# Optimization experiments

Hardware: AMD Instinct MI355X
Metric: run time of the kernel (lower is better)

Reference implementation:

```python
import jax, jax.numpy as jnp
import numpy as np

N_QUBITS = 8
REPS = 2
DIM = 2 ** N_QUBITS  # 256
C64 = jnp.complex64


def _apply_1q(state, gate, wire):
    """Apply a single-qubit gate. state: [B]+[2]*n, gate: [2,2] or [B,2,2]."""
    s = jnp.moveaxis(state, wire + 1, -1)
    if gate.ndim == 2:
        s = jnp.einsum('ij,b...j->b...i', gate, s)
    else:
        s = jnp.einsum('bij,b...j->b...i', gate, s)
    return jnp.moveaxis(s, -1, wire + 1)


def _cnot(state, ctrl, tgt):
    """CNOT: flip target axis where control bit == 1. state: [B]+[2]*n."""
    s0 = jax.lax.index_in_dim(state, 0, ctrl + 1, keepdims=True)
    s1 = jax.lax.index_in_dim(state, 1, ctrl + 1, keepdims=True)
    s1 = jnp.flip(s1, axis=tgt + 1)
    return jnp.concatenate([s0, s1], axis=ctrl + 1)


def _rx(a):
    """Batched RX gate. a: [B] -> [B,2,2] complex64."""
    c = jnp.cos(0.5 * a).astype(C64)
    s = jnp.sin(0.5 * a).astype(C64)
    mis = (-1j) * s
    return jnp.stack([jnp.stack([c, mis], -1), jnp.stack([mis, c], -1)], -2)


def _rot(phi, theta, omega):
    """PennyLane Rot = RZ(omega) RY(theta) RZ(phi). Scalars -> [2,2] complex64."""
    c = jnp.cos(0.5 * theta).astype(C64)
    s = jnp.sin(0.5 * theta).astype(C64)
    ep = jnp.exp(-0.5j * (phi + omega).astype(C64))   # e^{-i(phi+omega)/2}
    em = jnp.exp(-0.5j * (phi - omega).astype(C64))   # e^{-i(phi-omega)/2}
    epc = jnp.exp(0.5j * (phi + omega).astype(C64))
    emc = jnp.exp(0.5j * (phi - omega).astype(C64))
    return jnp.stack([
        jnp.stack([ep * c, -emc * s], -1),
        jnp.stack([em * s, epc * c], -1),
    ], -2)


def _circuit(x, theta):
    B = x.shape[0]
    state = jnp.zeros((B, DIM), C64).at[:, 0].set(1.0)
    state = state.reshape((B,) + (2,) * N_QUBITS)
    # AngleEmbedding (default rotation='X'): RX(x[:, w]) on wire w
    for w in range(N_QUBITS):
        state = _apply_1q(state, _rx(x[:, w]), w)
    # StronglyEntanglingLayers: per layer, Rot on every wire then ring of CNOTs
    for l in range(REPS):
        for w in range(N_QUBITS):
            g = _rot(theta[l, w, 0], theta[l, w, 1], theta[l, w, 2])
            state = _apply_1q(state, g, w)
        r = (l % (N_QUBITS - 1)) + 1  # PennyLane default ranges
        for w in range(N_QUBITS):
            state = _cnot(state, w, (w + r) % N_QUBITS)
    # expval(PauliZ(0)): wire 0 is the most significant axis
    probs = (state.real ** 2 + state.imag ** 2).reshape(B, 2, DIM // 2)
    ev = probs[:, 0].sum(-1) - probs[:, 1].sum(-1)
    return ((ev + 1.0) * 0.5)[:, None]  # [B, 1]


def setup_inputs() -> dict:
    key = jax.random.key(0)
    kx, kt = jax.random.split(key)
    x = jax.random.normal(kx, (131072, N_QUBITS), dtype=jnp.float32)
    theta = 0.1 * jax.random.normal(kt, (REPS, N_QUBITS, 3), dtype=jnp.float32)
    return {"x": x, "theta": theta}


def reference(x, theta):
    return _circuit(x, theta)
```

## Files before the change

### kernel.cpp

```cpp
#include <hip/hip_runtime.h>


typedef _Float16 v8hf __attribute__((ext_vector_type(8)));
typedef float v4f __attribute__((ext_vector_type(4)));

struct cpx { float re, im; };
__device__ __forceinline__ cpx cmul(cpx a, cpx b) {
    return {a.re * b.re - a.im * b.im, a.re * b.im + a.im * b.re};
}

__device__ __forceinline__ cpx pget(int a, int i, int j) {
    static const float RE[4][4] = {{1, 0, 0, 1}, {0, 1, 1, 0},
                                   {0, 0, 0, 0}, {1, 0, 0, -1}};
    static const float IM[4][4] = {{0, 0, 0, 0}, {0, 0, 0, 0},
                                   {0, -1, 1, 0}, {0, 0, 0, 0}};
    cpx r; r.re = RE[a][i * 2 + j]; r.im = IM[a][i * 2 + j];
    return r;
}

__device__ float ptm_entry(const float* __restrict__ theta, int g, int a, int b) {
    const int l = g >> 3, w = g & 7;
    const float phi = theta[(l * 8 + w) * 3 + 0];
    const float th  = theta[(l * 8 + w) * 3 + 1];
    const float om  = theta[(l * 8 + w) * 3 + 2];
    const float c = cosf(0.5f * th), s = sinf(0.5f * th);
    const float ps = 0.5f * (phi + om), ms = 0.5f * (phi - om);
    cpx G[2][2];
    G[0][0] = {c * cosf(ps), -c * sinf(ps)};
    G[0][1] = {-s * cosf(ms), -s * sinf(ms)};
    G[1][0] = {s * cosf(ms), -s * sinf(ms)};
    G[1][1] = {c * cosf(ps), c * sinf(ps)};
    cpx M1[2][2], H[2][2];
#pragma unroll
    for (int i = 0; i < 2; ++i)
#pragma unroll
        for (int j = 0; j < 2; ++j) {
            cpx acc{0.f, 0.f};
#pragma unroll
            for (int k = 0; k < 2; ++k) {
                cpx t = cmul(pget(a, i, k), G[k][j]);
                acc.re += t.re; acc.im += t.im;
            }
            M1[i][j] = acc;
        }
#pragma unroll
    for (int i = 0; i < 2; ++i)
#pragma unroll
        for (int j = 0; j < 2; ++j) {
            cpx acc{0.f, 0.f};
#pragma unroll
            for (int k = 0; k < 2; ++k) {
                cpx gc{G[k][i].re, -G[k][i].im};
                cpx t = cmul(gc, M1[k][j]);
                acc.re += t.re; acc.im += t.im;
            }
            H[i][j] = acc;
        }
    float tr = 0.f;
#pragma unroll
    for (int i = 0; i < 2; ++i)
#pragma unroll
        for (int j = 0; j < 2; ++j) {
            cpx pb = pget(b, i, j);
            tr += pb.re * H[j][i].re - pb.im * H[j][i].im;
        }
    return 0.5f * tr;
}

__device__ void cnot_entry(int pr, int cand, int* CIDX, float* CSGN) {
    const int pc = pr >> 2, pt = pr & 3;
    const int a = cand >> 2, b2 = cand & 3;
    const int perm[4] = {0, 1, 3, 2};
    float ov = 0.f;
#pragma unroll
    for (int r = 0; r < 4; ++r)
#pragma unroll
        for (int c2 = 0; c2 < 4; ++c2) {
            const int rp = perm[r], cp = perm[c2];
            cpx Rv = cmul(pget(pc, rp >> 1, cp >> 1), pget(pt, rp & 1, cp & 1));
            cpx Kv = cmul(pget(a, r >> 1, c2 >> 1), pget(b2, r & 1, c2 & 1));
            ov += Kv.re * Rv.re + Kv.im * Rv.im;
        }
    ov *= 0.25f;
    if (ov > 0.5f) { CIDX[pr] = cand; CSGN[pr] = 1.f; }
    else if (ov < -0.5f) { CIDX[pr] = cand; CSGN[pr] = -1.f; }
}

__device__ __forceinline__ int ring_conj_reg(int cur, int r,
                                             unsigned long long ci,
                                             unsigned cs, int& par) {
    for (int w = 7; w >= 0; --w) {
        const int tw = (w + r) & 7;
        const int pc = (cur >> (2 * w)) & 3;
        const int pt = (cur >> (2 * tw)) & 3;
        const int q = pc * 4 + pt;
        const int nq = (int)((ci >> (4 * q)) & 15ULL);
        par ^= (int)((cs >> q) & 1u);
        cur = (cur & ~((3 << (2 * w)) | (3 << (2 * tw))))
            | ((nq >> 2) << (2 * w)) | ((nq & 3) << (2 * tw));
    }
    return cur;
}

#define WS_FLOATS_NEEDED 6912

__global__ __launch_bounds__(1024) void k_prep4(const float* __restrict__ theta,
                                                float* __restrict__ ws) {
    _Float16* AF16 = (_Float16*)ws;
    const int tid = threadIdx.x;
    const int blk = blockIdx.x;

    if (blk == 9) {
        for (int h = tid; h < 27 * 64 * 8; h += 1024) {
            const int L = (h >> 3) & 63;
            const int jj = h & 7;
            const int m = L & 15;
            const int j = (L >> 4) * 8 + jj;
            const bool valid = (m < 12) && ((m & 3) < 3) && (j < 27);
            if (!valid) AF16[h] = (_Float16)0.f;
        }
        return;
    }

    __shared__ float Wa[4096];
    __shared__ float Wb[3072];
    __shared__ float TR[256];
    __shared__ float CSGN[16];
    __shared__ int   CIDX[16];
    __shared__ int   S1k, S1n;
    __shared__ float S1sgn;
    __shared__ int   S1w[8], S1l[8];

    const int P0 = blk / 3, P1 = blk % 3;
    const int let0 = (P0 == 0) ? 0 : ((P0 == 1) ? 3 : 2);
    const int let1 = (P1 == 0) ? 0 : ((P1 == 1) ? 3 : 2);

    if (tid < 256) TR[tid] = ptm_entry(theta, tid >> 4, (tid >> 2) & 3, tid & 3);
    else if (tid < 512) {
        const int r = tid - 256;
        cnot_entry(r >> 4, r & 15, CIDX, CSGN);
    }
    for (int i = tid; i < 4096; i += 1024) Wa[i] = 0.f;
    __syncthreads();

    unsigned long long cidx_pk = 0ULL;
    unsigned csgn_pk = 0u;
#pragma unroll
    for (int i2 = 0; i2 < 16; ++i2) {
        cidx_pk |= (unsigned long long)(CIDX[i2] & 15) << (4 * i2);
        csgn_pk |= (CSGN[i2] < 0.f ? 1u : 0u) << i2;
    }

    if (tid == 0) {
        int par = 0;
        int cur = ring_conj_reg(3 , 2, cidx_pk, csgn_pk, par);
        int k = 0;
        for (int w = 0; w < 8; ++w) {
            const int ltr = (cur >> (2 * w)) & 3;
            if (ltr != 0) { S1w[k] = w; S1l[k] = ltr; ++k; }
        }
        int n = 1;
        for (int i = 0; i < k; ++i) n *= 3;
        S1sgn = par ? -1.f : 1.f; S1k = k; S1n = n;
    }
    __syncthreads();
    const int k1 = S1k, n1 = S1n;

    for (int t = tid; t < n1; t += 1024) {
        float c = S1sgn;
        int s = 0;
        int tt = t;
        for (int i = 0; i < k1; ++i) {
            const int bl = tt % 3 + 1;
            tt /= 3;
            c *= TR[(8 + S1w[i]) * 16 + S1l[i] * 4 + bl];
            s |= bl << (2 * S1w[i]);
        }
        int par = 0;
        s = ring_conj_reg(s, 1, cidx_pk, csgn_pk, par);
        c = par ? -c : c;
        const int a0 = s & 3, a1 = (s >> 2) & 3;
        int d4 = 0;
#pragma unroll
        for (int w = 2; w < 8; ++w)
            d4 |= ((s >> (2 * w)) & 3) << (2 * (7 - w));
        const float v = c * TR[a0 * 4 + let0] * TR[16 + a1 * 4 + let1];
        atomicAdd(&Wa[d4], v);
    }
    __syncthreads();

    const int P3c[6] = {1, 3, 9, 27, 81, 243};
    const int N4c[6] = {1024, 256, 64, 16, 4, 1};
#pragma unroll
    for (int tl = 0; tl < 6; ++tl) {
        const int w = 7 - tl;
        const float* src = (tl & 1) ? Wb : Wa;
        float* dst = (tl & 1) ? Wa : Wb;
        const int p3 = P3c[tl];
        const int Nout = p3 * 3 * N4c[tl];
        for (int idx = tid; idx < Nout; idx += 1024) {
            const int q3 = idx % p3;
            const int rest = idx / p3;
            const int P = rest % 3;
            const int r = rest / 3;
            const int let = (P == 0) ? 0 : ((P == 1) ? 3 : 2);
            const float* ib = src + q3 + p3 * 4 * r;
            dst[idx] = ib[0] * TR[w * 16 + 0 + let]
                     + ib[p3] * TR[w * 16 + 4 + let]
                     + ib[2 * p3] * TR[w * 16 + 8 + let]
                     + ib[3 * p3] * TR[w * 16 + 12 + let];
        }
        __syncthreads();
    }

    const int m = 4 * P0 + P1;
    for (int idx = tid; idx < 729; idx += 1024) {
        const int T = idx / 27, j = idx % 27;
        const int h = (T * 64 + (j >> 3) * 16 + m) * 8 + (j & 7);
        AF16[h] = (_Float16)Wa[idx];
    }
}

__global__ __launch_bounds__(256) void k_main8(const float* __restrict__ x,
                                               const int* __restrict__ wsAF,
                                               float* __restrict__ out,
                                               int ngroups) {
    __shared__ int AFl[6912];
    const int tid = threadIdx.x;
    for (int u = tid; u < 6912; u += 256) AFl[u] = wsAF[u];
    __syncthreads();

    const int lane = tid & 63;
    const int q = lane >> 4, e = lane & 15;
    const bool q0b = (q == 0), q1b = (q == 1), q2b = (q == 2);
    const v8hf* AFp = (const v8hf*)AFl;
    const int wave = blockIdx.x * 4 + (tid >> 6);

#pragma unroll 1
    for (int gi = 0; gi < 2; ++gi) {
        const int g = wave * 2 + gi;
        if (g >= ngroups) break;
        const int b = g * 16 + e;
        const float4* xp = (const float4*)(x + (size_t)b * 8);
        const float4 xa = xp[0], xb = xp[1];

        float cw[8], msw[8];
        {
            const float xv[8] = {xa.x, xa.y, xa.z, xa.w, xb.x, xb.y, xb.z, xb.w};
#pragma unroll
            for (int w = 0; w < 8; ++w) {
                float sv, cv;
                __sincosf(xv[w], &sv, &cv);
                cw[w] = cv;
                msw[w] = -sv;
            }
        }

        float F2[27];
        {
            const float m5v[3] = {1.f, cw[5], msw[5]};
            const float m6v[3] = {1.f, cw[6], msw[6]};
            const float m7v[3] = {1.f, cw[7], msw[7]};
#pragma unroll
            for (int a = 0; a < 3; ++a)
#pragma unroll
                for (int b2 = 0; b2 < 3; ++b2) {
                    const float pp = m5v[a] * m6v[b2];
#pragma unroll
                    for (int c2 = 0; c2 < 3; ++c2)
                        F2[(a * 3 + b2) * 3 + c2] = pp * m7v[c2];
                }
        }
        v8hf bf;
#pragma unroll
        for (int jj = 0; jj < 8; ++jj) {
            const float c0 = F2[jj];
            const float c1 = F2[jj + 8];
            const float c2 = F2[jj + 16];
            const float c3 = (jj < 3) ? F2[jj + 24] : 0.f;
            const float v = q0b ? c0 : (q1b ? c1 : (q2b ? c2 : c3));
            bf[jj] = (_Float16)v;
        }

        const v4f zero = {0.f, 0.f, 0.f, 0.f};
        float h[9];
#pragma unroll
        for (int t = 0; t < 27; ++t) {
            const int a = t / 9, b2 = (t / 3) % 3, c2 = t % 3;
            v4f acc = __builtin_amdgcn_mfma_f32_16x16x32_f16(
                AFp[t * 64 + lane], bf, zero, 0, 0, 0);
            float f = fmaf(cw[1], acc[1], acc[0]);
            f = fmaf(msw[1], acc[2], f);
            if (c2 == 0)      h[a * 3 + b2] = f;
            else if (c2 == 1) h[a * 3 + b2] = fmaf(cw[4], f, h[a * 3 + b2]);
            else              h[a * 3 + b2] = fmaf(msw[4], f, h[a * 3 + b2]);
        }
        float e0 = fmaf(cw[3], h[1], h[0]); e0 = fmaf(msw[3], h[2], e0);
        float e1 = fmaf(cw[3], h[4], h[3]); e1 = fmaf(msw[3], h[5], e1);
        float e2 = fmaf(cw[3], h[7], h[6]); e2 = fmaf(msw[3], h[8], e2);
        float ev = fmaf(cw[2], e1, e0);
        ev = fmaf(msw[2], e2, ev);
        const float g0 = q0b ? 1.f : (q1b ? cw[0] : (q2b ? msw[0] : 0.f));
        ev *= g0;

        ev += __shfl_xor(ev, 16, 64);
        ev += __shfl_xor(ev, 32, 64);
        if (lane < 16) out[b] = (ev + 1.f) * 0.5f;
    }
}

struct c32 { float x, y; };

__device__ __forceinline__ c32 shfl_xor_c(c32 v, int mask) {
    c32 r;
    r.x = __shfl_xor(v.x, mask, 64);
    r.y = __shfl_xor(v.y, mask, 64);
    return r;
}
__device__ __forceinline__ c32 cmadd2(c32 ga, c32 a, c32 gp, c32 p) {
    c32 n;
    n.x = ga.x * a.x - ga.y * a.y + gp.x * p.x - gp.y * p.y;
    n.y = ga.x * a.y + ga.y * a.x + gp.x * p.y + gp.y * p.x;
    return n;
}
__device__ __forceinline__ c32 rx_mix(float c, float s, c32 a, c32 p) {
    c32 n;
    n.x = c * a.x + s * p.y;
    n.y = c * a.y - s * p.x;
    return n;
}
__device__ __forceinline__ void apply_rx(c32 st[4], int lane, int bb, float c, float s) {
    if (bb < 6) {
#pragma unroll
        for (int r = 0; r < 4; ++r) {
            c32 p = shfl_xor_c(st[r], 1 << bb);
            st[r] = rx_mix(c, s, st[r], p);
        }
    } else if (bb == 6) {
        c32 n0 = rx_mix(c, s, st[0], st[1]);
        c32 n1 = rx_mix(c, s, st[1], st[0]);
        c32 n2 = rx_mix(c, s, st[2], st[3]);
        c32 n3 = rx_mix(c, s, st[3], st[2]);
        st[0] = n0; st[1] = n1; st[2] = n2; st[3] = n3;
    } else {
        c32 n0 = rx_mix(c, s, st[0], st[2]);
        c32 n2 = rx_mix(c, s, st[2], st[0]);
        c32 n1 = rx_mix(c, s, st[1], st[3]);
        c32 n3 = rx_mix(c, s, st[3], st[1]);
        st[0] = n0; st[1] = n1; st[2] = n2; st[3] = n3;
    }
}
__device__ __forceinline__ void apply_rot(c32 st[4], int lane, int bb,
                                          c32 g00, c32 g01, c32 g10, c32 g11) {
    if (bb < 6) {
#pragma unroll
        for (int r = 0; r < 4; ++r) {
            c32 p = shfl_xor_c(st[r], 1 << bb);
            bool hi = (lane >> bb) & 1;
            c32 ga, gp;
            ga.x = hi ? g11.x : g00.x;
            ga.y = hi ? g11.y : g00.y;
            gp.x = hi ? g10.x : g01.x;
            gp.y = hi ? g10.y : g01.y;
            st[r] = cmadd2(ga, st[r], gp, p);
        }
    } else if (bb == 6) {
        c32 n0 = cmadd2(g00, st[0], g01, st[1]);
        c32 n1 = cmadd2(g10, st[0], g11, st[1]);
        c32 n2 = cmadd2(g00, st[2], g01, st[3]);
        c32 n3 = cmadd2(g10, st[2], g11, st[3]);
        st[0] = n0; st[1] = n1; st[2] = n2; st[3] = n3;
    } else {
        c32 n0 = cmadd2(g00, st[0], g01, st[2]);
        c32 n2 = cmadd2(g10, st[0], g11, st[2]);
        c32 n1 = cmadd2(g00, st[1], g01, st[3]);
        c32 n3 = cmadd2(g10, st[1], g11, st[3]);
        st[0] = n0; st[1] = n1; st[2] = n2; st[3] = n3;
    }
}
__device__ __forceinline__ void cswap(bool c, c32& a, c32& b) {
    c32 t = a;
    a.x = c ? b.x : a.x; a.y = c ? b.y : a.y;
    b.x = c ? t.x : b.x; b.y = c ? t.y : b.y;
}
__device__ __forceinline__ void apply_cnot(c32 st[4], int lane, int bc, int bt) {
    if (bt < 6) {
        if (bc < 6) {
            bool ctrl = (lane >> bc) & 1;
#pragma unroll
            for (int r = 0; r < 4; ++r) {
                c32 p = shfl_xor_c(st[r], 1 << bt);
                st[r].x = ctrl ? p.x : st[r].x;
                st[r].y = ctrl ? p.y : st[r].y;
            }
        } else {
#pragma unroll
            for (int r = 0; r < 4; ++r) {
                if ((r >> (bc - 6)) & 1) st[r] = shfl_xor_c(st[r], 1 << bt);
            }
        }
    } else {
        if (bc < 6) {
            bool ctrl = (lane >> bc) & 1;
            if (bt == 6) { cswap(ctrl, st[0], st[1]); cswap(ctrl, st[2], st[3]); }
            else         { cswap(ctrl, st[0], st[2]); cswap(ctrl, st[1], st[3]); }
        } else {
            if (bc == 7 && bt == 6) { c32 t = st[2]; st[2] = st[3]; st[3] = t; }
            else if (bc == 6 && bt == 7) { c32 t = st[1]; st[1] = st[3]; st[3] = t; }
        }
    }
}
__global__ __launch_bounds__(256) void qsim_kernel(const float* __restrict__ x,
                                                   const float* __restrict__ theta,
                                                   float* __restrict__ out,
                                                   int batch) {
    __shared__ float rot[2 * 8 * 8];
    const int t = threadIdx.x;
    if (t < 16) {
        const int l = t >> 3, w = t & 7;
        const float phi = theta[(l * 8 + w) * 3 + 0];
        const float th  = theta[(l * 8 + w) * 3 + 1];
        const float om  = theta[(l * 8 + w) * 3 + 2];
        const float c = cosf(0.5f * th), s = sinf(0.5f * th);
        const float p = 0.5f * (phi + om), m = 0.5f * (phi - om);
        float* g = &rot[t * 8];
        g[0] = c * cosf(p);  g[1] = -c * sinf(p);
        g[2] = -s * cosf(m); g[3] = -s * sinf(m);
        g[4] = s * cosf(m);  g[5] = -s * sinf(m);
        g[6] = c * cosf(p);  g[7] = c * sinf(p);
    }
    __syncthreads();
    const int lane = t & 63;
    const int b = blockIdx.x * 4 + (t >> 6);
    if (b >= batch) return;
    float c8 = 0.f, s8 = 0.f;
    if (lane < 8) {
        const float xv = 0.5f * x[b * 8 + lane];
        c8 = cosf(xv); s8 = sinf(xv);
    }
    c32 st[4];
#pragma unroll
    for (int r = 0; r < 4; ++r) { st[r].x = 0.f; st[r].y = 0.f; }
    if (lane == 0) st[0].x = 1.f;
#pragma unroll
    for (int w = 0; w < 8; ++w) {
        const float c = __shfl(c8, w, 64);
        const float s = __shfl(s8, w, 64);
        apply_rx(st, lane, 7 - w, c, s);
    }
#pragma unroll
    for (int l = 0; l < 2; ++l) {
#pragma unroll
        for (int w = 0; w < 8; ++w) {
            const float* g = &rot[(l * 8 + w) * 8];
            c32 g00{g[0], g[1]}, g01{g[2], g[3]}, g10{g[4], g[5]}, g11{g[6], g[7]};
            apply_rot(st, lane, 7 - w, g00, g01, g10, g11);
        }
        const int rr = l + 1;
#pragma unroll
        for (int w = 0; w < 8; ++w) apply_cnot(st, lane, 7 - w, 7 - ((w + rr) & 7));
    }
    float v = st[0].x * st[0].x + st[0].y * st[0].y
            + st[1].x * st[1].x + st[1].y * st[1].y
            - st[2].x * st[2].x - st[2].y * st[2].y
            - st[3].x * st[3].x - st[3].y * st[3].y;
#pragma unroll
    for (int off = 32; off > 0; off >>= 1) v += __shfl_xor(v, off, 64);
    if (lane == 0) out[b] = (v + 1.f) * 0.5f;
}

extern "C" void kernel_launch(void* const* d_in, const int* in_sizes, int n_in,
                              void* d_out, int out_size, void* d_ws, size_t ws_size,
                              hipStream_t stream) {
    const float* x     = (const float*)d_in[0];
    const float* theta = (const float*)d_in[1];
    float* out = (float*)d_out;
    const int batch = in_sizes[0] / 8;

    if (ws_size >= (size_t)WS_FLOATS_NEEDED * 4 + 256 && (batch & 15) == 0) {
        float* ws = (float*)d_ws;
        k_prep4<<<dim3(10), dim3(1024), 0, stream>>>(theta, ws);
        const int ngroups = batch / 16;
        const int blocks = (ngroups + 7) / 8;
        k_main8<<<dim3(blocks), dim3(256), 0, stream>>>(
            x, (const int*)ws, out, ngroups);
    } else {
        qsim_kernel<<<dim3((batch + 3) / 4), dim3(256), 0, stream>>>(x, theta, out, batch);
    }
}
```

Before: 69.21 us.

## Fuse prep and main kernels into one cooperative launch with grid sync

Merges the coefficient-prep kernel and the main MFMA kernel into a single cooperative kernel. The first ten blocks build the fp16 coefficient table, all blocks meet at a grid-wide sync, and then every block loads the table into LDS and processes its batch groups. The aim is to remove the second kernel launch and the gap between the two kernels. In exchange it relies on a cooperative launch with all 256 blocks of 1024 threads co-resident, adds grid-sync overhead, and uses larger blocks with more LDS each.

```diff
diff --git a/kernel.cpp b/kernel.cpp
--- a/kernel.cpp
+++ b/kernel.cpp
@@ -1,4 +1,7 @@
 #include <hip/hip_runtime.h>
+#include <hip/hip_cooperative_groups.h>
+
+namespace cg = cooperative_groups;
 
 
 typedef _Float16 v8hf __attribute__((ext_vector_type(8)));
@@ -104,33 +107,13 @@
 
 #define WS_FLOATS_NEEDED 6912
 
-__global__ __launch_bounds__(1024) void k_prep4(const float* __restrict__ theta,
-                                                float* __restrict__ ws) {
+__device__ __forceinline__ void prep_body(const float* __restrict__ theta,
+                                          float* __restrict__ ws, int blk,
+                                          int tid, float* Wa, float* Wb,
+                                          float* TR, float* CSGN, int* CIDX,
+                                          int* S1k, int* S1n, float* S1sgn,
+                                          int* S1w, int* S1l) {
     _Float16* AF16 = (_Float16*)ws;
-    const int tid = threadIdx.x;
-    const int blk = blockIdx.x;
-
-    if (blk == 9) {
-        for (int h = tid; h < 27 * 64 * 8; h += 1024) {
-            const int L = (h >> 3) & 63;
-            const int jj = h & 7;
-            const int m = L & 15;
-            const int j = (L >> 4) * 8 + jj;
-            const bool valid = (m < 12) && ((m & 3) < 3) && (j < 27);
-            if (!valid) AF16[h] = (_Float16)0.f;
-        }
-        return;
-    }
-
-    __shared__ float Wa[4096];
-    __shared__ float Wb[3072];
-    __shared__ float TR[256];
-    __shared__ float CSGN[16];
-    __shared__ int   CIDX[16];
-    __shared__ int   S1k, S1n;
-    __shared__ float S1sgn;
-    __shared__ int   S1w[8], S1l[8];
-
     const int P0 = blk / 3, P1 = blk % 3;
     const int let0 = (P0 == 0) ? 0 : ((P0 == 1) ? 3 : 2);
     const int let1 = (P1 == 0) ? 0 : ((P1 == 1) ? 3 : 2);
@@ -161,13 +144,13 @@
         }
         int n = 1;
         for (int i = 0; i < k; ++i) n *= 3;
-        S1sgn = par ? -1.f : 1.f; S1k = k; S1n = n;
+        *S1sgn = par ? -1.f : 1.f; *S1k = k; *S1n = n;
     }
     __syncthreads();
-    const int k1 = S1k, n1 = S1n;
+    const int k1 = *S1k, n1 = *S1n;
 
     for (int t = tid; t < n1; t += 1024) {
-        float c = S1sgn;
+        float c = *S1sgn;
         int s = 0;
         int tt = t;
         for (int i = 0; i < k1; ++i) {
@@ -221,6 +204,158 @@
     }
 }
 
+__device__ __forceinline__ void prep_zero_fill(float* __restrict__ ws, int tid,
+                                               int stride) {
+    _Float16* AF16 = (_Float16*)ws;
+    for (int h = tid; h < 27 * 64 * 8; h += stride) {
+        const int L = (h >> 3) & 63;
+        const int jj = h & 7;
+        const int m = L & 15;
+        const int j = (L >> 4) * 8 + jj;
+        const bool valid = (m < 12) && ((m & 3) < 3) && (j < 27);
+        if (!valid) AF16[h] = (_Float16)0.f;
+    }
+}
+
+__device__ __forceinline__ void main_group(const float* __restrict__ x,
+                                           float* __restrict__ out,
+                                           const v8hf* AFp, int b, int lane,
+                                           int q, bool q0b, bool q1b, bool q2b) {
+    const float4* xp = (const float4*)(x + (size_t)b * 8);
+    const float4 xa = xp[0], xb = xp[1];
+
+    float cw[8], msw[8];
+    {
+        const float xv[8] = {xa.x, xa.y, xa.z, xa.w, xb.x, xb.y, xb.z, xb.w};
+#pragma unroll
+        for (int w = 0; w < 8; ++w) {
+            float sv, cv;
+            __sincosf(xv[w], &sv, &cv);
+            cw[w] = cv;
+            msw[w] = -sv;
+        }
+    }
+
+    float F2[27];
+    {
+        const float m5v[3] = {1.f, cw[5], msw[5]};
+        const float m6v[3] = {1.f, cw[6], msw[6]};
+        const float m7v[3] = {1.f, cw[7], msw[7]};
+#pragma unroll
+        for (int a = 0; a < 3; ++a)
+#pragma unroll
+            for (int b2 = 0; b2 < 3; ++b2) {
+                const float pp = m5v[a] * m6v[b2];
+#pragma unroll
+                for (int c2 = 0; c2 < 3; ++c2)
+                    F2[(a * 3 + b2) * 3 + c2] = pp * m7v[c2];
+            }
+    }
+    v8hf bf;
+#pragma unroll
+    for (int jj = 0; jj < 8; ++jj) {
+        const float c0 = F2[jj];
+        const float c1 = F2[jj + 8];
+        const float c2 = F2[jj + 16];
+        const float c3 = (jj < 3) ? F2[jj + 24] : 0.f;
+        const float v = q0b ? c0 : (q1b ? c1 : (q2b ? c2 : c3));
+        bf[jj] = (_Float16)v;
+    }
+
+    const v4f zero = {0.f, 0.f, 0.f, 0.f};
+    float h[9];
+#pragma unroll
+    for (int t = 0; t < 27; ++t) {
+        const int a = t / 9, b2 = (t / 3) % 3, c2 = t % 3;
+        v4f acc = __builtin_amdgcn_mfma_f32_16x16x32_f16(
+            AFp[t * 64 + lane], bf, zero, 0, 0, 0);
+        float f = fmaf(cw[1], acc[1], acc[0]);
+        f = fmaf(msw[1], acc[2], f);
+        if (c2 == 0)      h[a * 3 + b2] = f;
+        else if (c2 == 1) h[a * 3 + b2] = fmaf(cw[4], f, h[a * 3 + b2]);
+        else              h[a * 3 + b2] = fmaf(msw[4], f, h[a * 3 + b2]);
+    }
+    float e0 = fmaf(cw[3], h[1], h[0]); e0 = fmaf(msw[3], h[2], e0);
+    float e1 = fmaf(cw[3], h[4], h[3]); e1 = fmaf(msw[3], h[5], e1);
+    float e2 = fmaf(cw[3], h[7], h[6]); e2 = fmaf(msw[3], h[8], e2);
+    float ev = fmaf(cw[2], e1, e0);
+    ev = fmaf(msw[2], e2, ev);
+    const float g0 = q0b ? 1.f : (q1b ? cw[0] : (q2b ? msw[0] : 0.f));
+    ev *= g0;
+
+    ev += __shfl_xor(ev, 16, 64);
+    ev += __shfl_xor(ev, 32, 64);
+    if (lane < 16) out[b] = (ev + 1.f) * 0.5f;
+}
+
+__global__ __launch_bounds__(1024, 4) void k_fused(const float* __restrict__ x,
+                                                   const float* __restrict__ theta,
+                                                   float* __restrict__ out,
+                                                   float* __restrict__ ws,
+                                                   int ngroups) {
+    __shared__ float Wa[4096];
+    __shared__ float Wb[3072];
+    __shared__ float TR[256];
+    __shared__ float CSGN[16];
+    __shared__ int   CIDX[16];
+    __shared__ int   S1k, S1n;
+    __shared__ float S1sgn;
+    __shared__ int   S1w[8], S1l[8];
+    __shared__ int   AFl[6912];
+
+    const int tid = threadIdx.x;
+    const int blk = blockIdx.x;
+
+    if (blk == 9) {
+        prep_zero_fill(ws, tid, 1024);
+    } else if (blk < 9) {
+        prep_body(theta, ws, blk, tid, Wa, Wb, TR, CSGN, CIDX,
+                  &S1k, &S1n, &S1sgn, S1w, S1l);
+    }
+
+    __threadfence();
+    cg::this_grid().sync();
+    __threadfence();
+
+    {
+        const int4* w4 = (const int4*)ws;
+        int4* a4 = (int4*)AFl;
+        for (int u = tid; u < 1728; u += 1024) a4[u] = w4[u];
+    }
+    __syncthreads();
+
+    const int lane = tid & 63;
+    const int q = lane >> 4, e = lane & 15;
+    const bool q0b = (q == 0), q1b = (q == 1), q2b = (q == 2);
+    const v8hf* AFp = (const v8hf*)AFl;
+    const int wave = blk * 16 + (tid >> 6);
+
+#pragma unroll 1
+    for (int gi = 0; gi < 2; ++gi) {
+        const int g = wave * 2 + gi;
+        if (g >= ngroups) break;
+        main_group(x, out, AFp, g * 16 + e, lane, q, q0b, q1b, q2b);
+    }
+}
+
+__global__ __launch_bounds__(1024) void k_prep4(const float* __restrict__ theta,
+                                                float* __restrict__ ws) {
+    const int tid = threadIdx.x;
+    const int blk = blockIdx.x;
+    if (blk == 9) { prep_zero_fill(ws, tid, 1024); return; }
+
+    __shared__ float Wa[4096];
+    __shared__ float Wb[3072];
+    __shared__ float TR[256];
+    __shared__ float CSGN[16];
+    __shared__ int   CIDX[16];
+    __shared__ int   S1k, S1n;
+    __shared__ float S1sgn;
+    __shared__ int   S1w[8], S1l[8];
+    prep_body(theta, ws, blk, tid, Wa, Wb, TR, CSGN, CIDX,
+              &S1k, &S1n, &S1sgn, S1w, S1l);
+}
+
 __global__ __launch_bounds__(256) void k_main8(const float* __restrict__ x,
                                                const int* __restrict__ wsAF,
                                                float* __restrict__ out,
@@ -240,72 +375,7 @@
     for (int gi = 0; gi < 2; ++gi) {
         const int g = wave * 2 + gi;
         if (g >= ngroups) break;
-        const int b = g * 16 + e;
-        const float4* xp = (const float4*)(x + (size_t)b * 8);
-        const float4 xa = xp[0], xb = xp[1];
-
-        float cw[8], msw[8];
-        {
-            const float xv[8] = {xa.x, xa.y, xa.z, xa.w, xb.x, xb.y, xb.z, xb.w};
-#pragma unroll
-            for (int w = 0; w < 8; ++w) {
-                float sv, cv;
-                __sincosf(xv[w], &sv, &cv);
-                cw[w] = cv;
-                msw[w] = -sv;
-            }
-        }
-
-        float F2[27];
-        {
-            const float m5v[3] = {1.f, cw[5], msw[5]};
-            const float m6v[3] = {1.f, cw[6], msw[6]};
-            const float m7v[3] = {1.f, cw[7], msw[7]};
-#pragma unroll
-            for (int a = 0; a < 3; ++a)
-#pragma unroll
-                for (int b2 = 0; b2 < 3; ++b2) {
-                    const float pp = m5v[a] * m6v[b2];
-#pragma unroll
-                    for (int c2 = 0; c2 < 3; ++c2)
-                        F2[(a * 3 + b2) * 3 + c2] = pp * m7v[c2];
-                }
-        }
-        v8hf bf;
-#pragma unroll
-        for (int jj = 0; jj < 8; ++jj) {
-            const float c0 = F2[jj];
-            const float c1 = F2[jj + 8];
-            const float c2 = F2[jj + 16];
-            const float c3 = (jj < 3) ? F2[jj + 24] : 0.f;
-            const float v = q0b ? c0 : (q1b ? c1 : (q2b ? c2 : c3));
-            bf[jj] = (_Float16)v;
-        }
-
-        const v4f zero = {0.f, 0.f, 0.f, 0.f};
-        float h[9];
-#pragma unroll
-        for (int t = 0; t < 27; ++t) {
-            const int a = t / 9, b2 = (t / 3) % 3, c2 = t % 3;
-            v4f acc = __builtin_amdgcn_mfma_f32_16x16x32_f16(
-                AFp[t * 64 + lane], bf, zero, 0, 0, 0);
-            float f = fmaf(cw[1], acc[1], acc[0]);
-            f = fmaf(msw[1], acc[2], f);
-            if (c2 == 0)      h[a * 3 + b2] = f;
-            else if (c2 == 1) h[a * 3 + b2] = fmaf(cw[4], f, h[a * 3 + b2]);
-            else              h[a * 3 + b2] = fmaf(msw[4], f, h[a * 3 + b2]);
-        }
-        float e0 = fmaf(cw[3], h[1], h[0]); e0 = fmaf(msw[3], h[2], e0);
-        float e1 = fmaf(cw[3], h[4], h[3]); e1 = fmaf(msw[3], h[5], e1);
-        float e2 = fmaf(cw[3], h[7], h[6]); e2 = fmaf(msw[3], h[8], e2);
-        float ev = fmaf(cw[2], e1, e0);
-        ev = fmaf(msw[2], e2, ev);
-        const float g0 = q0b ? 1.f : (q1b ? cw[0] : (q2b ? msw[0] : 0.f));
-        ev *= g0;
-
-        ev += __shfl_xor(ev, 16, 64);
-        ev += __shfl_xor(ev, 32, 64);
-        if (lane < 16) out[b] = (ev + 1.f) * 0.5f;
+        main_group(x, out, AFp, g * 16 + (tid & 15), lane, q, q0b, q1b, q2b);
     }
 }
 
@@ -479,11 +549,19 @@
 
     if (ws_size >= (size_t)WS_FLOATS_NEEDED * 4 + 256 && (batch & 15) == 0) {
         float* ws = (float*)d_ws;
-        k_prep4<<<dim3(10), dim3(1024), 0, stream>>>(theta, ws);
-        const int ngroups = batch / 16;
-        const int blocks = (ngroups + 7) / 8;
-        k_main8<<<dim3(blocks), dim3(256), 0, stream>>>(
-            x, (const int*)ws, out, ngroups);
+        int ngroups = batch / 16;
+        const int blocksM = (ngroups + 31) / 32;
+        if (blocksM >= 10 && blocksM <= 256) {
+            void* args[5] = {(void*)&x, (void*)&theta, (void*)&out,
+                             (void*)&ws, (void*)&ngroups};
+            hipLaunchCooperativeKernel((void*)k_fused, dim3(blocksM),
+                                       dim3(1024), args, 0, stream);
+        } else {
+            k_prep4<<<dim3(10), dim3(1024), 0, stream>>>(theta, ws);
+            const int blocks = (ngroups + 7) / 8;
+            k_main8<<<dim3(blocks), dim3(256), 0, stream>>>(
+                x, (const int*)ws, out, ngroups);
+        }
     } else {
         qsim_kernel<<<dim3((batch + 3) / 4), dim3(256), 0, stream>>>(x, theta, out, batch);
     }
```

After: 231.0 us. 234% more time.
